# Kernel optimization log

Hardware: AMD Instinct MI355X
Metric: run time of the kernel (lower is better)

The kernel has to match this reference:

```python
import jax, jax.numpy as jnp
import numpy as np

D_MODEL = 2048
N_HEADS = 16
HEAD_DIM = D_MODEL // N_HEADS  # 128


def setup_inputs() -> dict:
    key = jax.random.key(0)
    ks = jax.random.split(key, 7)
    B, S, CACHE = 2, 2048, 2048
    scale = 1.0 / np.sqrt(D_MODEL)
    return {
        "x": jax.random.normal(ks[0], (B, S, D_MODEL), dtype=jnp.float32),
        "cached_k": jax.random.normal(ks[1], (B, N_HEADS, CACHE, HEAD_DIM), dtype=jnp.float32),
        "cached_v": jax.random.normal(ks[2], (B, N_HEADS, CACHE, HEAD_DIM), dtype=jnp.float32),
        "W_q": jax.random.normal(ks[3], (D_MODEL, D_MODEL), dtype=jnp.float32) * scale,
        "W_k": jax.random.normal(ks[4], (D_MODEL, D_MODEL), dtype=jnp.float32) * scale,
        "W_v": jax.random.normal(ks[5], (D_MODEL, D_MODEL), dtype=jnp.float32) * scale,
        "W_o": jax.random.normal(ks[6], (D_MODEL, D_MODEL), dtype=jnp.float32) * scale,
    }


def reference(x, cached_k, cached_v, W_q, W_k, W_v, W_o):
    B, S, _ = x.shape
    # nn.Linear(d,d,bias=False): y = x @ W.T
    def proj(W):
        h = jnp.einsum("bsd,ed->bse", x, W)
        return h.reshape(B, S, N_HEADS, HEAD_DIM).transpose(0, 2, 1, 3)  # (B,H,S,Dh)
    q = proj(W_q)
    k = jnp.concatenate([cached_k, proj(W_k)], axis=2)  # (B,H,T,Dh)
    v = jnp.concatenate([cached_v, proj(W_v)], axis=2)
    scores = jnp.einsum("bhsd,bhtd->bhst", q, k) / np.sqrt(HEAD_DIM)
    attn = jax.nn.softmax(scores, axis=-1)
    out = jnp.einsum("bhst,bhtd->bhsd", attn, v)  # (B,H,S,Dh)
    out = out.transpose(0, 2, 1, 3).reshape(B, S, D_MODEL)
    out = jnp.einsum("bsd,ed->bse", out, W_o)
    return out, k, v
```

## Files before the change

kernel.cpp:

```cpp
#include <hip/hip_runtime.h>

typedef __bf16 bf16;
typedef __bf16 bf16x4 __attribute__((ext_vector_type(4)));
typedef __bf16 bf16x8 __attribute__((ext_vector_type(8)));
typedef float f32x4 __attribute__((ext_vector_type(4)));
typedef float f32x16 __attribute__((ext_vector_type(16)));
typedef int iv2 __attribute__((ext_vector_type(2)));

#define LOG2E 1.44269504088896340736f
#define QSCALE 0.12751884935f
#define RESCALE_THR 8.0f

__device__ __forceinline__ void gload_lds16(const void* gp, void* lp) {
    __builtin_amdgcn_global_load_lds(
        (__attribute__((address_space(1))) void*)gp,
        (__attribute__((address_space(3))) void*)lp,
        16, 0, 0);
}

__device__ __forceinline__ int kmask(int r) {
    return (r & 15) ^ (((r >> 5) & 1) << 2);
}

__device__ __forceinline__ unsigned cvtpk(float lo, float hi) {
    unsigned w;
    asm("v_cvt_pk_bf16_f32 %0, %1, %2" : "=v"(w) : "v"(lo), "v"(hi));
    return w;
}

__device__ __forceinline__ iv2 permswap(unsigned a, unsigned b) {
    return __builtin_amdgcn_permlane32_swap((int)a, (int)b, false, false);
}
__device__ __forceinline__ float halfmax(float v) {
    iv2 r = permswap(__float_as_uint(v), __float_as_uint(v));
    return fmaxf(__int_as_float(r[0]), __int_as_float(r[1]));
}
__device__ __forceinline__ float halfadd(float v) {
    iv2 r = permswap(__float_as_uint(v), __float_as_uint(v));
    return __int_as_float(r[0]) + __int_as_float(r[1]);
}

__device__ __forceinline__ float vmax32(const f32x16& a, const f32x16& b) {
    float t[8];
    #pragma unroll
    for (int i = 0; i < 8; ++i)
        t[i] = fmaxf(fmaxf(a[i], a[i + 8]), fmaxf(b[i], b[i + 8]));
    return fmaxf(fmaxf(fmaxf(t[0], t[1]), fmaxf(t[2], t[3])),
                 fmaxf(fmaxf(t[4], t[5]), fmaxf(t[6], t[7])));
}
__device__ __forceinline__ float vsum32(const f32x16& a, const f32x16& b) {
    float t[8];
    #pragma unroll
    for (int i = 0; i < 8; ++i)
        t[i] = (a[i] + a[i + 8]) + (b[i] + b[i + 8]);
    return ((t[0] + t[1]) + (t[2] + t[3])) + ((t[4] + t[5]) + (t[6] + t[7]));
}

__global__ void conv_all(const float* __restrict__ x, const float* __restrict__ wq,
                         const float* __restrict__ wk, const float* __restrict__ wv,
                         const float* __restrict__ wo, bf16* __restrict__ xb,
                         bf16* __restrict__ wbase) {
    int id = blockIdx.x;
    const float* src;
    bf16* dst;
    int i;
    if (id < 8192) {
        src = x; dst = xb;
        i = id * 256 + threadIdx.x;
    } else {
        int w = (id - 8192) >> 12;
        src = (w == 0) ? wq : (w == 1) ? wk : (w == 2) ? wv : wo;
        dst = wbase + (size_t)w * 4194304;
        i = ((id - 8192) & 4095) * 256 + threadIdx.x;
    }
    float4 f = ((const float4*)src)[i];
    bf16x4 v;
    v[0] = (bf16)f.x; v[1] = (bf16)f.y; v[2] = (bf16)f.z; v[3] = (bf16)f.w;
    *(bf16x4*)(dst + (size_t)i * 4) = v;
}

__global__ void copy_cache_k(const float* __restrict__ ck, float* __restrict__ kout,
                             bf16* __restrict__ kb) {
    size_t i = ((size_t)blockIdx.x * 256 + threadIdx.x) * 4;
    size_t bh  = i >> 18;
    size_t rem = i & 262143;
    size_t o   = (bh << 19) + rem;
    float4 f = *(const float4*)(ck + i);
    *(float4*)(kout + o) = f;
    bf16x4 v;
    v[0] = (bf16)f.x; v[1] = (bf16)f.y; v[2] = (bf16)f.z; v[3] = (bf16)f.w;
    *(bf16x4*)(kb + o) = v;
}

__global__ void copy_cache_v(const float* __restrict__ cv, float* __restrict__ vout,
                             bf16* __restrict__ vtb) {
    __shared__ float tile[32][33];
    int bh = blockIdx.z;
    int t0 = blockIdx.x * 32;
    int dh0 = blockIdx.y * 32;
    int tx = threadIdx.x, ty = threadIdx.y;
    const float* src = cv + (size_t)bh * 2048 * 128;
    float* dstf = vout + (size_t)bh * 4096 * 128;
    #pragma unroll
    for (int i = 0; i < 4; ++i) {
        int t = t0 + ty * 4 + i;
        float val = src[(size_t)t * 128 + dh0 + tx];
        dstf[(size_t)t * 128 + dh0 + tx] = val;
        tile[ty * 4 + i][tx] = val;
    }
    __syncthreads();
    bf16* dstb = vtb + (size_t)bh * 128 * 4096;
    #pragma unroll
    for (int i = 0; i < 4; ++i) {
        int dh = dh0 + ty * 4 + i;
        dstb[(size_t)dh * 4096 + t0 + tx] = (bf16)tile[tx][ty * 4 + i];
    }
}

__global__ __launch_bounds__(256)
void gemm_qkv(const bf16* __restrict__ A, const bf16* __restrict__ Bm,
              float* __restrict__ kout, float* __restrict__ vout,
              bf16* __restrict__ qb, bf16* __restrict__ kb, bf16* __restrict__ vtb) {
    const int K = 2048;
    __shared__ __align__(16) char smem[32768];
    const int tid = threadIdx.x;
    const int wid = tid >> 6;
    const int lane = tid & 63;
    const int quad = lane >> 4;
    const int l16 = lane & 15;
    const int wg = blockIdx.x;
    const int wgid = (wg & 7) * 192 + (wg >> 3);
    const int m0 = (wgid / 48) * 128;
    const int n0 = (wgid % 48) * 128;
    const int wm = (wid & 1) * 64;
    const int wn = (wid >> 1) * 64;

    f32x4 zero = {0.f, 0.f, 0.f, 0.f};
    f32x4 acc[4][4];
    #pragma unroll
    for (int i = 0; i < 4; ++i)
        #pragma unroll
        for (int j = 0; j < 4; ++j) acc[i][j] = zero;

    auto stage = [&](int k0, int buf) {
        char* base = smem + buf * 16384;
        #pragma unroll
        for (int t = 0; t < 2; ++t) {
            int c = t * 256 + tid;
            int row = c >> 2, kc = c & 3;
            const char* gA = (const char*)(A + (size_t)(m0 + row) * K + k0 + kc * 8);
            const char* gB = (const char*)(Bm + (size_t)(n0 + row) * K + k0 + kc * 8);
            char* lA = base + (size_t)(t * 256 + (tid & ~63)) * 16;
            char* lB = base + 8192 + (size_t)(t * 256 + (tid & ~63)) * 16;
            gload_lds16(gA, lA);
            gload_lds16(gB, lB);
        }
    };

    stage(0, 0);
    __syncthreads();

    for (int k0 = 0; k0 < K; k0 += 32) {
        const int cur = (k0 >> 5) & 1;
        if (k0 + 32 < K) stage(k0 + 32, cur ^ 1);
        const char* base = smem + cur * 16384;
        bf16x8 af[4], bfv[4];
        #pragma unroll
        for (int i = 0; i < 4; ++i) {
            af[i]  = *(const bf16x8*)(base + ((wm + i * 16 + l16) * 32 + quad * 8) * 2);
            bfv[i] = *(const bf16x8*)(base + 8192 + ((wn + i * 16 + l16) * 32 + quad * 8) * 2);
        }
        __builtin_amdgcn_s_setprio(1);
        #pragma unroll
        for (int i = 0; i < 4; ++i)
            #pragma unroll
            for (int j = 0; j < 4; ++j)
                acc[i][j] = __builtin_amdgcn_mfma_f32_16x16x32_bf16(af[i], bfv[j], acc[i][j], 0, 0, 0);
        __builtin_amdgcn_s_setprio(0);
        __syncthreads();
    }

    const int seg = n0 >> 11;
    #pragma unroll
    for (int i = 0; i < 4; ++i)
        #pragma unroll
        for (int j = 0; j < 4; ++j)
            #pragma unroll
            for (int r = 0; r < 4; ++r) {
                int grow = m0 + wm + i * 16 + quad * 4 + r;
                int gcol = n0 + wn + j * 16 + l16;
                float v = acc[i][j][r];
                int b = grow >> 11, s = grow & 2047;
                int c2 = gcol & 2047;
                int h = c2 >> 7, dh = c2 & 127;
                if (seg == 0) {
                    qb[(((size_t)(b * 16 + h) * 2048) + s) * 128 + dh] = (bf16)(v * QSCALE);
                } else if (seg == 1) {
                    size_t idx = (((size_t)(b * 16 + h) * 4096) + 2048 + s) * 128 + dh;
                    kout[idx] = v;
                    kb[idx] = (bf16)v;
                } else {
                    size_t idx = (((size_t)(b * 16 + h) * 4096) + 2048 + s) * 128 + dh;
                    vout[idx] = v;
                    vtb[(((size_t)(b * 16 + h) * 128) + dh) * 4096 + 2048 + s] = (bf16)v;
                }
            }
}

__global__ __launch_bounds__(256)
void gemm_out(const bf16* __restrict__ A, const bf16* __restrict__ Bm,
              float* __restrict__ out_f32) {
    const int K = 2048, N = 2048;
    __shared__ __align__(16) char smem[32768];
    const int tid = threadIdx.x;
    const int wid = tid >> 6;
    const int lane = tid & 63;
    const int quad = lane >> 4;
    const int l16 = lane & 15;
    const int wg = blockIdx.x;
    const int wgid = (wg & 7) * 64 + (wg >> 3);
    const int m0 = (wgid >> 4) * 128;
    const int n0 = (wgid & 15) * 128;
    const int wm = (wid & 1) * 64;
    const int wn = (wid >> 1) * 64;

    f32x4 zero = {0.f, 0.f, 0.f, 0.f};
    f32x4 acc[4][4];
    #pragma unroll
    for (int i = 0; i < 4; ++i)
        #pragma unroll
        for (int j = 0; j < 4; ++j) acc[i][j] = zero;

    auto stage = [&](int k0, int buf) {
        char* base = smem + buf * 16384;
        #pragma unroll
        for (int t = 0; t < 2; ++t) {
            int c = t * 256 + tid;
            int row = c >> 2, kc = c & 3;
            const char* gA = (const char*)(A + (size_t)(m0 + row) * K + k0 + kc * 8);
            const char* gB = (const char*)(Bm + (size_t)(n0 + row) * K + k0 + kc * 8);
            char* lA = base + (size_t)(t * 256 + (tid & ~63)) * 16;
            char* lB = base + 8192 + (size_t)(t * 256 + (tid & ~63)) * 16;
            gload_lds16(gA, lA);
            gload_lds16(gB, lB);
        }
    };

    stage(0, 0);
    __syncthreads();

    for (int k0 = 0; k0 < K; k0 += 32) {
        const int cur = (k0 >> 5) & 1;
        if (k0 + 32 < K) stage(k0 + 32, cur ^ 1);
        const char* base = smem + cur * 16384;
        bf16x8 af[4], bfv[4];
        #pragma unroll
        for (int i = 0; i < 4; ++i) {
            af[i]  = *(const bf16x8*)(base + ((wm + i * 16 + l16) * 32 + quad * 8) * 2);
            bfv[i] = *(const bf16x8*)(base + 8192 + ((wn + i * 16 + l16) * 32 + quad * 8) * 2);
        }
        __builtin_amdgcn_s_setprio(1);
        #pragma unroll
        for (int i = 0; i < 4; ++i)
            #pragma unroll
            for (int j = 0; j < 4; ++j)
                acc[i][j] = __builtin_amdgcn_mfma_f32_16x16x32_bf16(af[i], bfv[j], acc[i][j], 0, 0, 0);
        __builtin_amdgcn_s_setprio(0);
        __syncthreads();
    }

    #pragma unroll
    for (int i = 0; i < 4; ++i)
        #pragma unroll
        for (int j = 0; j < 4; ++j)
            #pragma unroll
            for (int r = 0; r < 4; ++r) {
                int grow = m0 + wm + i * 16 + quad * 4 + r;
                int gcol = n0 + wn + j * 16 + l16;
                out_f32[(size_t)grow * N + gcol] = acc[i][j][r];
            }
}

__global__ __launch_bounds__(256, 2)
void flash_attn(const bf16* __restrict__ qb, const bf16* __restrict__ kb,
                const bf16* __restrict__ vtb, bf16* __restrict__ ab) {
    __shared__ __align__(16) char smem[65536];
    const int tid = threadIdx.x;
    const int wid = tid >> 6;
    const int lane = tid & 63;
    const int hh = lane >> 5;
    const int l31 = lane & 31;

    const int flat = blockIdx.x;
    const int xcd = flat & 7;
    const int idx = flat >> 3;
    const int bh = xcd * 4 + (idx >> 4);
    const int qblk = idx & 15;
    const int b = bh >> 4, h = bh & 15;
    const int s0 = qblk * 128 + wid * 32;

    const bf16* Q  = qb  + (size_t)bh * 2048 * 128;
    const bf16* Kp = kb  + (size_t)bh * 4096 * 128;
    const bf16* Vt = vtb + (size_t)bh * 128 * 4096;

    bf16x8 qf[8];
    #pragma unroll
    for (int ks = 0; ks < 8; ++ks)
        qf[ks] = *(const bf16x8*)(Q + (size_t)(s0 + l31) * 128 + ks * 16 + hh * 8);

    f32x16 oacc[4];
    #pragma unroll
    for (int dhb = 0; dhb < 4; ++dhb)
        #pragma unroll
        for (int i = 0; i < 16; ++i) oacc[dhb][i] = 0.f;
    float mrun = -1e30f, lrun = 0.f;

    auto stage = [&](int t0, int buf) {
        char* Kb = smem + buf * 32768;
        char* Vb = Kb + 16384;
        #pragma unroll
        for (int r4 = 0; r4 < 4; ++r4) {
            int kc = r4 * 256 + tid;
            int row = kc >> 4, p = kc & 15;
            int j = p ^ kmask(row);
            gload_lds16(Kp + (size_t)(t0 + row) * 128 + j * 8, Kb + kc * 16);
        }
        #pragma unroll
        for (int r4 = 0; r4 < 4; ++r4) {
            int vc = r4 * 256 + tid;
            int row = vc >> 4, j = vc & 15;
            int g = j ^ kmask(row);
            int dh = row + (g >> 3) * 64;
            int p = g & 7;
            gload_lds16(Vt + (size_t)dh * 4096 + t0 + p * 8, Vb + vc * 16);
        }
    };

    stage(0, 0);
    __syncthreads();

    for (int t0 = 0; t0 < 4096; t0 += 64) {
        const int cur = (t0 >> 6) & 1;
        if (t0 + 64 < 4096) stage(t0 + 64, cur ^ 1);
        const char* Ksh = smem + cur * 32768;
        const char* Vsh = Ksh + 16384;

        f32x16 sacc[2];
        #pragma unroll
        for (int i = 0; i < 16; ++i) { sacc[0][i] = 0.f; sacc[1][i] = 0.f; }
        __builtin_amdgcn_s_setprio(1);
        #pragma unroll
        for (int ks = 0; ks < 8; ++ks) {
            const int c = ks * 2 + hh;
            const int r0 = l31, r1 = 32 + l31;
            bf16x8 kf0 = *(const bf16x8*)(Ksh + r0 * 256 + (c ^ kmask(r0)) * 16);
            bf16x8 kf1 = *(const bf16x8*)(Ksh + r1 * 256 + (c ^ kmask(r1)) * 16);
            sacc[0] = __builtin_amdgcn_mfma_f32_32x32x16_bf16(kf0, qf[ks], sacc[0], 0, 0, 0);
            sacc[1] = __builtin_amdgcn_mfma_f32_32x32x16_bf16(kf1, qf[ks], sacc[1], 0, 0, 0);
        }
        __builtin_amdgcn_s_setprio(0);

        float mx = halfmax(vmax32(sacc[0], sacc[1]));
        if (!__all(mx <= mrun + RESCALE_THR)) {
            float mnew = fmaxf(mrun, mx);
            float alpha = __builtin_amdgcn_exp2f(mrun - mnew);
            #pragma unroll
            for (int dhb = 0; dhb < 4; ++dhb)
                #pragma unroll
                for (int i = 0; i < 16; ++i) oacc[dhb][i] *= alpha;
            lrun *= alpha;
            mrun = mnew;
        }
        #pragma unroll
        for (int tb = 0; tb < 2; ++tb)
            #pragma unroll
            for (int i = 0; i < 16; ++i)
                sacc[tb][i] = __builtin_amdgcn_exp2f(sacc[tb][i] - mrun);
        lrun += halfadd(vsum32(sacc[0], sacc[1]));

        bf16x8 pf[4];
        #pragma unroll
        for (int tb = 0; tb < 2; ++tb)
            #pragma unroll
            for (int ksl = 0; ksl < 2; ++ksl) {
                const int g0 = ksl * 8;
                unsigned wa0 = cvtpk(sacc[tb][g0 + 0], sacc[tb][g0 + 1]);
                unsigned wb0 = cvtpk(sacc[tb][g0 + 4], sacc[tb][g0 + 5]);
                unsigned wa1 = cvtpk(sacc[tb][g0 + 2], sacc[tb][g0 + 3]);
                unsigned wb1 = cvtpk(sacc[tb][g0 + 6], sacc[tb][g0 + 7]);
                iv2 r0 = permswap(wa0, wb0);
                iv2 r1 = permswap(wa1, wb1);
                union { int u[4]; bf16x8 v; } pk;
                pk.u[0] = r0[0]; pk.u[1] = r1[0]; pk.u[2] = r0[1]; pk.u[3] = r1[1];
                pf[tb * 2 + ksl] = pk.v;
            }

        __builtin_amdgcn_s_setprio(1);
        #pragma unroll
        for (int dhb = 0; dhb < 4; ++dhb) {
            const int rr = ((dhb & 1) << 5) + l31;
            #pragma unroll
            for (int ks = 0; ks < 4; ++ks) {
                const int g = (dhb >> 1) * 8 + ks * 2 + hh;
                bf16x8 vf = *(const bf16x8*)(Vsh + rr * 256 + (g ^ kmask(rr)) * 16);
                oacc[dhb] = __builtin_amdgcn_mfma_f32_32x32x16_bf16(vf, pf[ks], oacc[dhb], 0, 0, 0);
            }
        }
        __builtin_amdgcn_s_setprio(0);

        __syncthreads();
    }

    const float inv = 1.0f / lrun;
    const int s = s0 + l31;
    #pragma unroll
    for (int dhb = 0; dhb < 4; ++dhb)
        #pragma unroll
        for (int g = 0; g < 4; ++g) {
            bf16x4 o4;
            #pragma unroll
            for (int r = 0; r < 4; ++r) o4[r] = (bf16)(oacc[dhb][g * 4 + r] * inv);
            int dh = dhb * 32 + g * 8 + hh * 4;
            *(bf16x4*)(ab + ((size_t)(b * 2048 + s)) * 2048 + h * 128 + dh) = o4;
        }
}

extern "C" void kernel_launch(void* const* d_in, const int* in_sizes, int n_in,
                              void* d_out, int out_size, void* d_ws, size_t ws_size,
                              hipStream_t stream) {
    const float* x        = (const float*)d_in[0];
    const float* cached_k = (const float*)d_in[1];
    const float* cached_v = (const float*)d_in[2];
    const float* W_q      = (const float*)d_in[3];
    const float* W_k      = (const float*)d_in[4];
    const float* W_v      = (const float*)d_in[5];
    const float* W_o      = (const float*)d_in[6];

    float* out  = (float*)d_out;
    float* kout = out + 8388608;
    float* vout = out + 25165824;

    char* ws = (char*)d_ws;
    size_t off = 0;
    auto alloc = [&](size_t elts) { bf16* p = (bf16*)(ws + off); off += elts * 2; return p; };
    bf16* xb  = alloc(8388608);
    bf16* wqb = alloc(4194304);
    bf16* wkb = alloc(4194304);
    bf16* wvb = alloc(4194304);
    bf16* wob = alloc(4194304);
    bf16* qb  = alloc(8388608);
    bf16* kb  = alloc(16777216);
    bf16* vtb = alloc(16777216);
    bf16* ab  = alloc(8388608);
    (void)wkb; (void)wvb;

    conv_all<<<24576, 256, 0, stream>>>(x, W_q, W_k, W_v, W_o, xb, wqb);
    copy_cache_k<<<8192, 256, 0, stream>>>(cached_k, kout, kb);
    copy_cache_v<<<dim3(64, 4, 32), dim3(32, 8), 0, stream>>>(cached_v, vout, vtb);

    gemm_qkv<<<1536, 256, 0, stream>>>(xb, wqb, kout, vout, qb, kb, vtb);

    flash_attn<<<512, 256, 0, stream>>>(qb, kb, vtb, ab);

    gemm_out<<<512, 256, 0, stream>>>(ab, wob, out);
}
```

Baseline: 650.6 us.

## Move V-transpose out of QKV GEMM epilogue and remap workgroups per XCD

Removes the strided scattered bf16 store of transposed V from the QKV GEMM epilogue and adds a separate tiled transpose kernel that reads the fp32 V output back and writes the transposed bf16 copy with coalesced stores. Both GEMMs also change their workgroup-to-tile mapping so each XCD owns a contiguous band of N columns across all M rows, instead of a strided swizzle. This aims to cut uncoalesced write traffic and improve L2 locality of weight tiles per XCD. The cost is an extra kernel launch plus an extra read of the new V half, and the new mapping may reduce reuse of A tiles.

```diff
diff --git a/kernel.cpp b/kernel.cpp
--- a/kernel.cpp
+++ b/kernel.cpp
@@ -117,10 +117,31 @@
     }
 }
 
+__global__ void transpose_vnew(const float* __restrict__ vout, bf16* __restrict__ vtb) {
+    __shared__ float tile[32][33];
+    int bh = blockIdx.z;
+    int t0 = 2048 + blockIdx.x * 32;
+    int dh0 = blockIdx.y * 32;
+    int tx = threadIdx.x, ty = threadIdx.y;
+    const float* src = vout + (size_t)bh * 4096 * 128;
+    #pragma unroll
+    for (int i = 0; i < 4; ++i) {
+        int t = t0 + ty * 4 + i;
+        tile[ty * 4 + i][tx] = src[(size_t)t * 128 + dh0 + tx];
+    }
+    __syncthreads();
+    bf16* dstb = vtb + (size_t)bh * 128 * 4096;
+    #pragma unroll
+    for (int i = 0; i < 4; ++i) {
+        int dh = dh0 + ty * 4 + i;
+        dstb[(size_t)dh * 4096 + t0 + tx] = (bf16)tile[tx][ty * 4 + i];
+    }
+}
+
 __global__ __launch_bounds__(256)
 void gemm_qkv(const bf16* __restrict__ A, const bf16* __restrict__ Bm,
               float* __restrict__ kout, float* __restrict__ vout,
-              bf16* __restrict__ qb, bf16* __restrict__ kb, bf16* __restrict__ vtb) {
+              bf16* __restrict__ qb, bf16* __restrict__ kb) {
     const int K = 2048;
     __shared__ __align__(16) char smem[32768];
     const int tid = threadIdx.x;
@@ -129,9 +150,10 @@
     const int quad = lane >> 4;
     const int l16 = lane & 15;
     const int wg = blockIdx.x;
-    const int wgid = (wg & 7) * 192 + (wg >> 3);
-    const int m0 = (wgid / 48) * 128;
-    const int n0 = (wgid % 48) * 128;
+    const int xcd = wg & 7;
+    const int i_x = wg >> 3;
+    const int m0 = (i_x / 6) * 128;
+    const int n0 = (xcd * 6 + i_x % 6) * 128;
     const int wm = (wid & 1) * 64;
     const int wn = (wid >> 1) * 64;
 
@@ -150,7 +172,7 @@
             int row = c >> 2, kc = c & 3;
             const char* gA = (const char*)(A + (size_t)(m0 + row) * K + k0 + kc * 8);
             const char* gB = (const char*)(Bm + (size_t)(n0 + row) * K + k0 + kc * 8);
-            char* lA = base + (size_t)(t * 256 + (tid & ~63)) * 16;
+            char* lA = smem + buf * 16384 + (size_t)(t * 256 + (tid & ~63)) * 16;
             char* lB = base + 8192 + (size_t)(t * 256 + (tid & ~63)) * 16;
             gload_lds16(gA, lA);
             gload_lds16(gB, lB);
@@ -202,7 +224,6 @@
                 } else {
                     size_t idx = (((size_t)(b * 16 + h) * 4096) + 2048 + s) * 128 + dh;
                     vout[idx] = v;
-                    vtb[(((size_t)(b * 16 + h) * 128) + dh) * 4096 + 2048 + s] = (bf16)v;
                 }
             }
 }
@@ -218,9 +239,10 @@
     const int quad = lane >> 4;
     const int l16 = lane & 15;
     const int wg = blockIdx.x;
-    const int wgid = (wg & 7) * 64 + (wg >> 3);
-    const int m0 = (wgid >> 4) * 128;
-    const int n0 = (wgid & 15) * 128;
+    const int xcd = wg & 7;
+    const int i_x = wg >> 3;
+    const int m0 = (i_x >> 1) * 128;
+    const int n0 = (xcd * 2 + (i_x & 1)) * 128;
     const int wm = (wid & 1) * 64;
     const int wn = (wid >> 1) * 64;
 
@@ -458,7 +480,8 @@
     copy_cache_k<<<8192, 256, 0, stream>>>(cached_k, kout, kb);
     copy_cache_v<<<dim3(64, 4, 32), dim3(32, 8), 0, stream>>>(cached_v, vout, vtb);
 
-    gemm_qkv<<<1536, 256, 0, stream>>>(xb, wqb, kout, vout, qb, kb, vtb);
+    gemm_qkv<<<1536, 256, 0, stream>>>(xb, wqb, kout, vout, qb, kb);
+    transpose_vnew<<<dim3(64, 4, 32), dim3(32, 8), 0, stream>>>(vout, vtb);
 
     flash_attn<<<512, 256, 0, stream>>>(qb, kb, vtb, ab);
 
```

Measured after the change: 642.0 us. Within noise of the previous version (-1.3%).
